# Optimization experiments

Hardware: AMD Instinct MI355X
Metric: run time of the kernel (lower is better)

## Reference

```python
import jax, jax.numpy as jnp
import numpy as np

IN_FEATURES = 2048
OUT_FEATURES = 2048
LOG_DIM = 11                      # ceil(log2(2048))
BUTTERFLY_DIM = 2 ** LOG_DIM      # 2048
MAX_BLOCKS = BUTTERFLY_DIM // 2   # 1024 (layer 0 has the most blocks)
BATCH = 16384


def setup_inputs() -> dict:
    key = jax.random.key(0)
    ks = jax.random.split(key, 5)
    x = jax.random.normal(ks[0], (BATCH, IN_FEATURES), dtype=jnp.float32)
    # Linear weights stored torch-style: [out, in]
    w_in = jax.random.normal(ks[1], (BUTTERFLY_DIM, IN_FEATURES), dtype=jnp.float32) * 0.02
    w_out = jax.random.normal(ks[2], (OUT_FEATURES, BUTTERFLY_DIM), dtype=jnp.float32) * 0.02
    b_out = jnp.zeros((OUT_FEATURES,), dtype=jnp.float32)
    # Per-stage rotation params: theta = rand*0.01, a=cos(theta), b=sin(theta).
    # Stage l uses num_blocks = BUTTERFLY_DIM // 2^(l+1) entries; pad to MAX_BLOCKS.
    theta = jax.random.uniform(ks[3], (LOG_DIM, MAX_BLOCKS), dtype=jnp.float32) * 0.01
    a_pad = jnp.cos(theta)
    b_pad = jnp.sin(theta)
    return {"x": x, "w_in": w_in, "w_out": w_out, "b_out": b_out,
            "a_pad": a_pad, "b_pad": b_pad}


def _butterfly(x, a_pad, b_pad):
    # x: [B, BUTTERFLY_DIM]
    B = x.shape[0]
    for l in range(LOG_DIM):
        block_size = 2 ** l
        num_blocks = BUTTERFLY_DIM // (2 * block_size)
        a = a_pad[l, :num_blocks][None, :, None]  # [1, nb, 1]
        b = b_pad[l, :num_blocks][None, :, None]
        xv = x.reshape(B, num_blocks, 2, block_size)
        x0 = xv[:, :, 0, :]
        x1 = xv[:, :, 1, :]
        top = a * x0 + b * x1
        bot = -b * x0 + a * x1
        x = jnp.stack([top, bot], axis=2).reshape(B, BUTTERFLY_DIM)
    return x


def reference(x, w_in, w_out, b_out, a_pad, b_pad):
    h = x @ w_in.T                      # [B, BUTTERFLY_DIM]
    h = _butterfly(h, a_pad, b_pad)
    return h @ w_out.T + b_out          # [B, OUT_FEATURES]
```

## Files before the change

kernel.cpp:

```cpp
#include <hip/hip_runtime.h>
#include <hip/hip_bf16.h>

using bf16 = __hip_bfloat16;
using bf16x8 = __attribute__((ext_vector_type(8))) __bf16;
using f32x4 = __attribute__((ext_vector_type(4))) float;

typedef const __attribute__((address_space(1))) void* gas_ptr;
typedef __attribute__((address_space(3))) void* las_ptr;
#define LOAD_LDS16(g, l) \
    __builtin_amdgcn_global_load_lds((gas_ptr)(const void*)(g), (las_ptr)(void*)(l), 16, 0, 0)

#define LOG_DIM 11
#define BDIM 2048
#define NFEAT 2048
#define BATCH 16384

__global__ __launch_bounds__(256) void cvt_fp32_bf16(const float* __restrict__ in,
                                                     bf16* __restrict__ out) {
    size_t i = ((size_t)blockIdx.x * 256 + threadIdx.x) * 8;
    float4 v0 = *(const float4*)(in + i);
    float4 v1 = *(const float4*)(in + i + 4);
    union { bf16 h[8]; int4 v; } u;
    u.h[0] = __float2bfloat16(v0.x); u.h[1] = __float2bfloat16(v0.y);
    u.h[2] = __float2bfloat16(v0.z); u.h[3] = __float2bfloat16(v0.w);
    u.h[4] = __float2bfloat16(v1.x); u.h[5] = __float2bfloat16(v1.y);
    u.h[6] = __float2bfloat16(v1.z); u.h[7] = __float2bfloat16(v1.w);
    *(int4*)(out + i) = u.v;
}

__global__ __launch_bounds__(256) void butterfly_wout(const float* __restrict__ W,
                                                      const float* __restrict__ a_pad,
                                                      const float* __restrict__ b_pad,
                                                      bf16* __restrict__ out) {
    __shared__ float v[BDIM];
    const int o = blockIdx.x;
    const int t = threadIdx.x;
    const float* row = W + (size_t)o * BDIM;
    for (int i = t; i < BDIM / 4; i += 256)
        ((float4*)v)[i] = ((const float4*)row)[i];
    __syncthreads();
    for (int l = LOG_DIM - 1; l >= 0; --l) {
        const int bs = 1 << l;
        #pragma unroll
        for (int pp = 0; pp < 4; ++pp) {
            int p = t + pp * 256;
            int j = p >> l;
            int s = p & (bs - 1);
            int i0 = (j << (l + 1)) | s;
            int i1 = i0 + bs;
            float a = a_pad[l * (BDIM / 2) + j];
            float b = b_pad[l * (BDIM / 2) + j];
            float x0 = v[i0], x1 = v[i1];
            v[i0] = a * x0 - b * x1;
            v[i1] = b * x0 + a * x1;
        }
        __syncthreads();
    }
    union { bf16 h[8]; int4 vv; } u;
    #pragma unroll
    for (int j = 0; j < 8; ++j) u.h[j] = __float2bfloat16(v[t * 8 + j]);
    *(int4*)(out + (size_t)o * BDIM + t * 8) = u.vv;
}

__global__ __launch_bounds__(256) void transpose_cvt(const float* __restrict__ in,
                                                     bf16* __restrict__ out) {
    __shared__ float tile[32][33];
    const int bx = blockIdx.x, by = blockIdx.y;
    const int tx = threadIdx.x & 31, ty = threadIdx.x >> 5;
    #pragma unroll
    for (int r = ty; r < 32; r += 8)
        tile[r][tx] = in[(size_t)(by * 32 + r) * NFEAT + bx * 32 + tx];
    __syncthreads();
    #pragma unroll
    for (int r = ty; r < 32; r += 8)
        out[(size_t)(bx * 32 + r) * NFEAT + by * 32 + tx] = __float2bfloat16(tile[tx][r]);
}

__global__ __launch_bounds__(256, 2) void gemm_bt_splitk(const bf16* __restrict__ A,
                                                         const bf16* __restrict__ Bt,
                                                         bf16* __restrict__ Cpart) {
    constexpr int BM = 128, BN = 128, BK = 32;
    constexpr int LDA = 2048, KLEN = 512, NN = 2048;
    __shared__ bf16 sA[BM * BK];
    __shared__ bf16 sB[BN * BK];

    const int kz = blockIdx.z;
    A += kz * KLEN;
    Bt += kz * KLEN;
    bf16* C = Cpart + (size_t)kz * NN * NN;

    const int tid = threadIdx.x;
    const int wave = tid >> 6;
    const int lane = tid & 63;
    const int wr = wave >> 1;
    const int wc = wave & 1;

    const int mBase = blockIdx.y * BM;
    const int nBase = blockIdx.x * BN;

    const int r0 = tid >> 2, c0 = tid & 3;
    const int r1 = (256 + tid) >> 2;

    const bf16* gA0 = A + (size_t)(mBase + r0) * LDA + c0 * 8;
    const bf16* gA1 = A + (size_t)(mBase + r1) * LDA + c0 * 8;
    const bf16* gB0 = Bt + (size_t)(nBase + r0) * LDA + c0 * 8;
    const bf16* gB1 = Bt + (size_t)(nBase + r1) * LDA + c0 * 8;

    char* lA0 = (char*)sA + (wave * 64) * 16;
    char* lA1 = (char*)sA + (256 + wave * 64) * 16;
    char* lB0 = (char*)sB + (wave * 64) * 16;
    char* lB1 = (char*)sB + (256 + wave * 64) * 16;

    f32x4 acc[4][4];
    #pragma unroll
    for (int i = 0; i < 4; ++i)
        #pragma unroll
        for (int j = 0; j < 4; ++j) acc[i][j] = (f32x4){0.f, 0.f, 0.f, 0.f};

    const int aRow = wr * 64 + (lane & 15);
    const int bRow = wc * 64 + (lane & 15);
    const int kOff = (lane >> 4) * 8;

    for (int k0 = 0; k0 < KLEN; k0 += BK) {
        LOAD_LDS16(gA0, lA0);
        LOAD_LDS16(gA1, lA1);
        LOAD_LDS16(gB0, lB0);
        LOAD_LDS16(gB1, lB1);
        gA0 += BK; gA1 += BK; gB0 += BK; gB1 += BK;
        __syncthreads();

        bf16x8 af[4], bfr[4];
        #pragma unroll
        for (int mf = 0; mf < 4; ++mf)
            af[mf] = *reinterpret_cast<const bf16x8*>(&sA[(aRow + mf * 16) * BK + kOff]);
        #pragma unroll
        for (int nf = 0; nf < 4; ++nf)
            bfr[nf] = *reinterpret_cast<const bf16x8*>(&sB[(bRow + nf * 16) * BK + kOff]);
        #pragma unroll
        for (int mf = 0; mf < 4; ++mf)
            #pragma unroll
            for (int nf = 0; nf < 4; ++nf)
                acc[mf][nf] = __builtin_amdgcn_mfma_f32_16x16x32_bf16(
                    af[mf], bfr[nf], acc[mf][nf], 0, 0, 0);
        __syncthreads();
    }

    const int cRow0 = mBase + wr * 64 + (lane >> 4) * 4;
    const int cCol0 = nBase + wc * 64 + (lane & 15);
    #pragma unroll
    for (int mf = 0; mf < 4; ++mf)
        #pragma unroll
        for (int nf = 0; nf < 4; ++nf)
            #pragma unroll
            for (int r = 0; r < 4; ++r)
                C[(size_t)(cRow0 + mf * 16 + r) * NN + cCol0 + nf * 16] =
                    __float2bfloat16(acc[mf][nf][r]);
}

__global__ __launch_bounds__(256) void addcvt4(const bf16* __restrict__ p,
                                               bf16* __restrict__ out) {
    size_t i = ((size_t)blockIdx.x * 256 + threadIdx.x) * 8;
    constexpr size_t STRIDE = (size_t)2048 * 2048;
    float s[8];
    #pragma unroll
    for (int j = 0; j < 8; ++j) s[j] = 0.f;
    #pragma unroll
    for (int z = 0; z < 4; ++z) {
        union { bf16 h[8]; int4 v; } a;
        a.v = *(const int4*)(p + z * STRIDE + i);
        #pragma unroll
        for (int j = 0; j < 8; ++j) s[j] += __bfloat162float(a.h[j]);
    }
    union { bf16 h[8]; int4 v; } o;
    #pragma unroll
    for (int j = 0; j < 8; ++j) o.h[j] = __float2bfloat16(s[j]);
    *(int4*)(out + i) = o.v;
}

#define GK 2048
#define LDS_SLOT 65536
#define LDS_BOFF 32768
#define LDS_KH 16384

__global__ __launch_bounds__(512, 2) void gemm256(const bf16* __restrict__ A,
                                                  const bf16* __restrict__ Bt,
                                                  const float* __restrict__ bias,
                                                  float* __restrict__ C) {
    __shared__ __align__(16) char lds[131072];

    const int tid = threadIdx.x;
    const int wave = tid >> 6, lane = tid & 63;
    const int l15 = lane & 15, kc = lane >> 4;
    const int wm = wave >> 2, wn = wave & 3;

    const int bid = blockIdx.x;
    const int swz = (bid & 7) * 64 + (bid >> 3);
    const int bm = swz >> 3, bn = swz & 7;
    const int mBase = bm * 256, nBase = bn * 256;

    const int c_log = tid ^ ((tid >> 3) & 3);
    const int srow = c_log >> 2, skc = c_log & 3;
    const bf16* gA = A + (size_t)(mBase + srow) * GK + skc * 8;
    const bf16* gB = Bt + (size_t)(nBase + srow) * GK + skc * 8;
    const int stgBase = wave * 1024;

    const int kcx = kc ^ ((l15 >> 1) & 3);
    const int aoff = wm * 8192 + l15 * 64 + kcx * 16;
    const int boff = LDS_BOFF + wn * 4096 + l15 * 64 + kcx * 16;

    f32x4 acc[8][4];
    #pragma unroll
    for (int i = 0; i < 8; ++i)
        #pragma unroll
        for (int j = 0; j < 4; ++j) acc[i][j] = (f32x4){0.f, 0.f, 0.f, 0.f};
    bf16x8 bfr[4];

#define STG(GSRC, LDSC, KT, KH) do {                                        \
    const bf16* _g = (GSRC) + (KT) * 64 + (KH) * 32;                        \
    LOAD_LDS16(_g, lds + (LDSC) + stgBase);                                 \
    LOAD_LDS16(_g + (size_t)128 * GK, lds + (LDSC) + stgBase + 8192);       \
} while (0)

    STG(gA, 0 * LDS_SLOT + 0, 0, 0);
    STG(gB, 0 * LDS_SLOT + LDS_BOFF + 0, 0, 0);
    STG(gA, 0 * LDS_SLOT + LDS_KH, 0, 1);
    STG(gB, 0 * LDS_SLOT + LDS_BOFF + LDS_KH, 0, 1);
    STG(gA, 1 * LDS_SLOT + 0, 1, 0);
    STG(gB, 1 * LDS_SLOT + LDS_BOFF + 0, 1, 0);
    STG(gB, 1 * LDS_SLOT + LDS_BOFF + LDS_KH, 1, 1);
    asm volatile("s_waitcnt vmcnt(6)");
    __builtin_amdgcn_s_barrier();

#define PHASE(SLOT, KH, MH, SGSRC, SLDS, SKT, SKH, DOVM) do {               \
    const int _rb = (SLOT) * LDS_SLOT + (KH) * LDS_KH;                      \
    bf16x8 _a[4];                                                           \
    _Pragma("unroll")                                                       \
    for (int _mf = 0; _mf < 4; ++_mf)                                       \
        _a[_mf] = *(const bf16x8*)(lds + _rb + aoff + (MH) * 4096 + _mf * 1024); \
    if (!(MH)) {                                                            \
        _Pragma("unroll")                                                   \
        for (int _nf = 0; _nf < 4; ++_nf)                                   \
            bfr[_nf] = *(const bf16x8*)(lds + _rb + boff + _nf * 1024);     \
    }                                                                       \
    STG(SGSRC, SLDS, SKT, SKH);                                             \
    if (DOVM) asm volatile("s_waitcnt vmcnt(6)");                           \
    __builtin_amdgcn_s_barrier();                                           \
    asm volatile("s_waitcnt lgkmcnt(0)");                                   \
    __builtin_amdgcn_s_setprio(1);                                          \
    _Pragma("unroll")                                                       \
    for (int _mf = 0; _mf < 4; ++_mf)                                       \
        _Pragma("unroll")                                                   \
        for (int _nf = 0; _nf < 4; ++_nf)                                   \
            acc[(MH) * 4 + _mf][_nf] = __builtin_amdgcn_mfma_f32_16x16x32_bf16( \
                _a[_mf], bfr[_nf], acc[(MH) * 4 + _mf][_nf], 0, 0, 0);      \
    __builtin_amdgcn_s_setprio(0);                                          \
    __builtin_amdgcn_s_barrier();                                           \
} while (0)

    for (int it = 0; it < 16; ++it) {
        const int t0 = 2 * it;
        const int t1 = (t0 + 1) & 31, t2 = (t0 + 2) & 31, t3 = (t0 + 3) & 31;
        PHASE(0, 0, 0, gA, 1 * LDS_SLOT + LDS_KH,            t1, 1, 0);
        PHASE(0, 0, 1, gB, 0 * LDS_SLOT + LDS_BOFF,          t2, 0, 0);
        PHASE(0, 1, 0, gA, 0 * LDS_SLOT + 0,                 t2, 0, 0);
        PHASE(0, 1, 1, gB, 0 * LDS_SLOT + LDS_BOFF + LDS_KH, t2, 1, 1);
        PHASE(1, 0, 0, gA, 0 * LDS_SLOT + LDS_KH,            t2, 1, 0);
        PHASE(1, 0, 1, gB, 1 * LDS_SLOT + LDS_BOFF,          t3, 0, 0);
        PHASE(1, 1, 0, gA, 1 * LDS_SLOT + 0,                 t3, 0, 0);
        PHASE(1, 1, 1, gB, 1 * LDS_SLOT + LDS_BOFF + LDS_KH, t3, 1, 1);
    }

    const int cRow0 = mBase + wm * 128 + (lane >> 4) * 4;
    const int cCol0 = nBase + wn * 64 + l15;
    float bv[4];
    #pragma unroll
    for (int nf = 0; nf < 4; ++nf) bv[nf] = bias[cCol0 + nf * 16];
    #pragma unroll
    for (int Mf = 0; Mf < 8; ++Mf)
        #pragma unroll
        for (int nf = 0; nf < 4; ++nf)
            #pragma unroll
            for (int r = 0; r < 4; ++r)
                C[(size_t)(cRow0 + Mf * 16 + r) * GK + cCol0 + nf * 16] =
                    acc[Mf][nf][r] + bv[nf];
#undef PHASE
#undef STG
}

extern "C" void kernel_launch(void* const* d_in, const int* in_sizes, int n_in,
                              void* d_out, int out_size, void* d_ws, size_t ws_size,
                              hipStream_t stream) {
    const float* x     = (const float*)d_in[0];
    const float* w_in  = (const float*)d_in[1];
    const float* w_out = (const float*)d_in[2];
    const float* b_out = (const float*)d_in[3];
    const float* a_pad = (const float*)d_in[4];
    const float* b_pad = (const float*)d_in[5];
    float* out = (float*)d_out;

    char* ws = (char*)d_ws;
    bf16* x_bf  = (bf16*)ws;
    bf16* woutb = (bf16*)(ws + (size_t)67108864);
    bf16* wint  = (bf16*)(ws + (size_t)75497472);
    bf16* mcomb = (bf16*)(ws + (size_t)83886080);

    bf16* part = (bf16*)d_out;

    cvt_fp32_bf16<<<dim3(BATCH * NFEAT / (256 * 8)), dim3(256), 0, stream>>>(x, x_bf);
    butterfly_wout<<<dim3(NFEAT), dim3(256), 0, stream>>>(w_out, a_pad, b_pad, woutb);
    transpose_cvt<<<dim3(NFEAT / 32, BDIM / 32), dim3(256), 0, stream>>>(w_in, wint);
    gemm_bt_splitk<<<dim3(NFEAT / 128, BDIM / 128, 4), dim3(256), 0, stream>>>(
        woutb, wint, part);
    addcvt4<<<dim3(NFEAT * BDIM / (256 * 8)), dim3(256), 0, stream>>>(part, mcomb);
    gemm256<<<dim3((BATCH / 256) * (NFEAT / 256)), dim3(512), 0, stream>>>(
        x_bf, mcomb, b_out, out);
}
```

Before: 223.7 us.

## Merge prep kernels and double-buffer LDS fragment reads in main GEMM

The butterfly-on-w_out and w_in transpose kernels are merged into one launch, and the x fp32-to-bf16 conversion is interleaved with the split-K weight GEMM in a second launch. This cuts launch count and lets the memory-bound conversion overlap with the compute-bound small GEMM. The main 256x256 GEMM now reads the next phase's A/B fragments from LDS into alternate register sets while the current MFMAs run, removing the lgkmcnt(0) stall before each MFMA block. This adds register pressure and relies on barrier placement to keep the prefetched LDS reads valid.

```diff
diff --git a/kernel.cpp b/kernel.cpp
--- a/kernel.cpp
+++ b/kernel.cpp
@@ -15,88 +15,91 @@
 #define NFEAT 2048
 #define BATCH 16384
 
-__global__ __launch_bounds__(256) void cvt_fp32_bf16(const float* __restrict__ in,
-                                                     bf16* __restrict__ out) {
-    size_t i = ((size_t)blockIdx.x * 256 + threadIdx.x) * 8;
-    float4 v0 = *(const float4*)(in + i);
-    float4 v1 = *(const float4*)(in + i + 4);
-    union { bf16 h[8]; int4 v; } u;
-    u.h[0] = __float2bfloat16(v0.x); u.h[1] = __float2bfloat16(v0.y);
-    u.h[2] = __float2bfloat16(v0.z); u.h[3] = __float2bfloat16(v0.w);
-    u.h[4] = __float2bfloat16(v1.x); u.h[5] = __float2bfloat16(v1.y);
-    u.h[6] = __float2bfloat16(v1.z); u.h[7] = __float2bfloat16(v1.w);
-    *(int4*)(out + i) = u.v;
-}
-
-__global__ __launch_bounds__(256) void butterfly_wout(const float* __restrict__ W,
-                                                      const float* __restrict__ a_pad,
-                                                      const float* __restrict__ b_pad,
-                                                      bf16* __restrict__ out) {
+__global__ __launch_bounds__(256) void prep1(const float* __restrict__ w_out,
+                                             const float* __restrict__ a_pad,
+                                             const float* __restrict__ b_pad,
+                                             const float* __restrict__ w_in,
+                                             bf16* __restrict__ woutb,
+                                             bf16* __restrict__ wint) {
     __shared__ float v[BDIM];
-    const int o = blockIdx.x;
+    __shared__ float tile[32][33];
     const int t = threadIdx.x;
-    const float* row = W + (size_t)o * BDIM;
-    for (int i = t; i < BDIM / 4; i += 256)
-        ((float4*)v)[i] = ((const float4*)row)[i];
-    __syncthreads();
-    for (int l = LOG_DIM - 1; l >= 0; --l) {
-        const int bs = 1 << l;
-        #pragma unroll
-        for (int pp = 0; pp < 4; ++pp) {
-            int p = t + pp * 256;
-            int j = p >> l;
-            int s = p & (bs - 1);
-            int i0 = (j << (l + 1)) | s;
-            int i1 = i0 + bs;
-            float a = a_pad[l * (BDIM / 2) + j];
-            float b = b_pad[l * (BDIM / 2) + j];
-            float x0 = v[i0], x1 = v[i1];
-            v[i0] = a * x0 - b * x1;
-            v[i1] = b * x0 + a * x1;
+    if (blockIdx.x < 2048) {
+        const int o = blockIdx.x;
+        const float* row = w_out + (size_t)o * BDIM;
+        for (int i = t; i < BDIM / 4; i += 256)
+            ((float4*)v)[i] = ((const float4*)row)[i];
+        __syncthreads();
+        for (int l = LOG_DIM - 1; l >= 0; --l) {
+            #pragma unroll
+            for (int pp = 0; pp < 4; ++pp) {
+                int p = t + pp * 256;
+                int j = p >> l;
+                int s = p & ((1 << l) - 1);
+                int i0 = (j << (l + 1)) | s;
+                int i1 = i0 + (1 << l);
+                float a = a_pad[l * (BDIM / 2) + j];
+                float b = b_pad[l * (BDIM / 2) + j];
+                float x0 = v[i0], x1 = v[i1];
+                v[i0] = a * x0 - b * x1;
+                v[i1] = b * x0 + a * x1;
+            }
+            __syncthreads();
         }
+        union { bf16 h[8]; int4 vv; } u;
+        #pragma unroll
+        for (int j = 0; j < 8; ++j) u.h[j] = __float2bfloat16(v[t * 8 + j]);
+        *(int4*)(woutb + (size_t)o * BDIM + t * 8) = u.vv;
+    } else {
+        const int b = blockIdx.x - 2048;
+        const int bx = b & 63, by = b >> 6;
+        const int tx = t & 31, ty = t >> 5;
+        #pragma unroll
+        for (int r = ty; r < 32; r += 8)
+            tile[r][tx] = w_in[(size_t)(by * 32 + r) * NFEAT + bx * 32 + tx];
         __syncthreads();
-    }
-    union { bf16 h[8]; int4 vv; } u;
-    #pragma unroll
-    for (int j = 0; j < 8; ++j) u.h[j] = __float2bfloat16(v[t * 8 + j]);
-    *(int4*)(out + (size_t)o * BDIM + t * 8) = u.vv;
-}
-
-__global__ __launch_bounds__(256) void transpose_cvt(const float* __restrict__ in,
-                                                     bf16* __restrict__ out) {
-    __shared__ float tile[32][33];
-    const int bx = blockIdx.x, by = blockIdx.y;
-    const int tx = threadIdx.x & 31, ty = threadIdx.x >> 5;
-    #pragma unroll
-    for (int r = ty; r < 32; r += 8)
-        tile[r][tx] = in[(size_t)(by * 32 + r) * NFEAT + bx * 32 + tx];
-    __syncthreads();
-    #pragma unroll
-    for (int r = ty; r < 32; r += 8)
-        out[(size_t)(bx * 32 + r) * NFEAT + by * 32 + tx] = __float2bfloat16(tile[tx][r]);
-}
-
-__global__ __launch_bounds__(256, 2) void gemm_bt_splitk(const bf16* __restrict__ A,
-                                                         const bf16* __restrict__ Bt,
-                                                         bf16* __restrict__ Cpart) {
-    constexpr int BM = 128, BN = 128, BK = 32;
-    constexpr int LDA = 2048, KLEN = 512, NN = 2048;
-    __shared__ bf16 sA[BM * BK];
-    __shared__ bf16 sB[BN * BK];
-
-    const int kz = blockIdx.z;
-    A += kz * KLEN;
-    Bt += kz * KLEN;
+        #pragma unroll
+        for (int r = ty; r < 32; r += 8)
+            wint[(size_t)(bx * 32 + r) * NFEAT + by * 32 + tx] = __float2bfloat16(tile[tx][r]);
+    }
+}
+
+__global__ __launch_bounds__(256, 2) void prep2(const bf16* __restrict__ Aw,
+                                                const bf16* __restrict__ Btw,
+                                                bf16* __restrict__ Cpart,
+                                                const float* __restrict__ x,
+                                                bf16* __restrict__ x_bf) {
+    __shared__ bf16 sA[128 * 32];
+    __shared__ bf16 sB[128 * 32];
+    const int tid = threadIdx.x;
+
+    if (blockIdx.x & 1) {
+        const int vb = blockIdx.x >> 1;
+        #pragma unroll
+        for (int it = 0; it < 16; ++it) {
+            size_t i = ((size_t)vb * 16 + it) * 2048 + tid * 8;
+            float4 v0 = *(const float4*)(x + i);
+            float4 v1 = *(const float4*)(x + i + 4);
+            union { bf16 h[8]; int4 v; } u;
+            u.h[0] = __float2bfloat16(v0.x); u.h[1] = __float2bfloat16(v0.y);
+            u.h[2] = __float2bfloat16(v0.z); u.h[3] = __float2bfloat16(v0.w);
+            u.h[4] = __float2bfloat16(v1.x); u.h[5] = __float2bfloat16(v1.y);
+            u.h[6] = __float2bfloat16(v1.z); u.h[7] = __float2bfloat16(v1.w);
+            *(int4*)(x_bf + i) = u.v;
+        }
+        return;
+    }
+
+    constexpr int BK = 32, LDA = 2048, KLEN = 512, NN = 2048;
+    const int sk = blockIdx.x >> 1;
+    const int bx = sk & 15, by = (sk >> 4) & 15, kz = sk >> 8;
+    const bf16* A = Aw + kz * KLEN;
+    const bf16* Bt = Btw + kz * KLEN;
     bf16* C = Cpart + (size_t)kz * NN * NN;
 
-    const int tid = threadIdx.x;
-    const int wave = tid >> 6;
-    const int lane = tid & 63;
-    const int wr = wave >> 1;
-    const int wc = wave & 1;
-
-    const int mBase = blockIdx.y * BM;
-    const int nBase = blockIdx.x * BN;
+    const int wave = tid >> 6, lane = tid & 63;
+    const int wr = wave >> 1, wc = wave & 1;
+    const int mBase = by * 128, nBase = bx * 128;
 
     const int r0 = tid >> 2, c0 = tid & 3;
     const int r1 = (256 + tid) >> 2;
@@ -128,7 +131,6 @@
         LOAD_LDS16(gB1, lB1);
         gA0 += BK; gA1 += BK; gB0 += BK; gB1 += BK;
         __syncthreads();
-
         bf16x8 af[4], bfr[4];
         #pragma unroll
         for (int mf = 0; mf < 4; ++mf)
@@ -213,12 +215,25 @@
     for (int i = 0; i < 8; ++i)
         #pragma unroll
         for (int j = 0; j < 4; ++j) acc[i][j] = (f32x4){0.f, 0.f, 0.f, 0.f};
-    bf16x8 bfr[4];
+
+    bf16x8 Aa[4], Ab[4], Ba[4], Bb[4];
 
 #define STG(GSRC, LDSC, KT, KH) do {                                        \
     const bf16* _g = (GSRC) + (KT) * 64 + (KH) * 32;                        \
     LOAD_LDS16(_g, lds + (LDSC) + stgBase);                                 \
     LOAD_LDS16(_g + (size_t)128 * GK, lds + (LDSC) + stgBase + 8192);       \
+} while (0)
+
+#define READP(AN, BN, SLOT, KH, MH, DOB) do {                               \
+    const int _rb = (SLOT) * LDS_SLOT + (KH) * LDS_KH;                      \
+    _Pragma("unroll")                                                       \
+    for (int _f = 0; _f < 4; ++_f)                                          \
+        AN[_f] = *(const bf16x8*)(lds + _rb + aoff + (MH) * 4096 + _f * 1024); \
+    if (DOB) {                                                              \
+        _Pragma("unroll")                                                   \
+        for (int _f = 0; _f < 4; ++_f)                                      \
+            BN[_f] = *(const bf16x8*)(lds + _rb + boff + _f * 1024);        \
+    }                                                                       \
 } while (0)
 
     STG(gA, 0 * LDS_SLOT + 0, 0, 0);
@@ -230,29 +245,20 @@
     STG(gB, 1 * LDS_SLOT + LDS_BOFF + LDS_KH, 1, 1);
     asm volatile("s_waitcnt vmcnt(6)");
     __builtin_amdgcn_s_barrier();
-
-#define PHASE(SLOT, KH, MH, SGSRC, SLDS, SKT, SKH, DOVM) do {               \
-    const int _rb = (SLOT) * LDS_SLOT + (KH) * LDS_KH;                      \
-    bf16x8 _a[4];                                                           \
-    _Pragma("unroll")                                                       \
-    for (int _mf = 0; _mf < 4; ++_mf)                                       \
-        _a[_mf] = *(const bf16x8*)(lds + _rb + aoff + (MH) * 4096 + _mf * 1024); \
-    if (!(MH)) {                                                            \
-        _Pragma("unroll")                                                   \
-        for (int _nf = 0; _nf < 4; ++_nf)                                   \
-            bfr[_nf] = *(const bf16x8*)(lds + _rb + boff + _nf * 1024);     \
-    }                                                                       \
+    READP(Aa, Ba, 0, 0, 0, 1);
+
+#define PH(CURA, CURB, NXTA, NXTB, MH, RS, RKH, RMH, RDOB, SGSRC, SLDS, SKT, SKH, DOVM) do { \
     STG(SGSRC, SLDS, SKT, SKH);                                             \
     if (DOVM) asm volatile("s_waitcnt vmcnt(6)");                           \
     __builtin_amdgcn_s_barrier();                                           \
-    asm volatile("s_waitcnt lgkmcnt(0)");                                   \
+    READP(NXTA, NXTB, RS, RKH, RMH, RDOB);                                  \
     __builtin_amdgcn_s_setprio(1);                                          \
     _Pragma("unroll")                                                       \
     for (int _mf = 0; _mf < 4; ++_mf)                                       \
         _Pragma("unroll")                                                   \
         for (int _nf = 0; _nf < 4; ++_nf)                                   \
             acc[(MH) * 4 + _mf][_nf] = __builtin_amdgcn_mfma_f32_16x16x32_bf16( \
-                _a[_mf], bfr[_nf], acc[(MH) * 4 + _mf][_nf], 0, 0, 0);      \
+                CURA[_mf], CURB[_nf], acc[(MH) * 4 + _mf][_nf], 0, 0, 0);   \
     __builtin_amdgcn_s_setprio(0);                                          \
     __builtin_amdgcn_s_barrier();                                           \
 } while (0)
@@ -260,14 +266,14 @@
     for (int it = 0; it < 16; ++it) {
         const int t0 = 2 * it;
         const int t1 = (t0 + 1) & 31, t2 = (t0 + 2) & 31, t3 = (t0 + 3) & 31;
-        PHASE(0, 0, 0, gA, 1 * LDS_SLOT + LDS_KH,            t1, 1, 0);
-        PHASE(0, 0, 1, gB, 0 * LDS_SLOT + LDS_BOFF,          t2, 0, 0);
-        PHASE(0, 1, 0, gA, 0 * LDS_SLOT + 0,                 t2, 0, 0);
-        PHASE(0, 1, 1, gB, 0 * LDS_SLOT + LDS_BOFF + LDS_KH, t2, 1, 1);
-        PHASE(1, 0, 0, gA, 0 * LDS_SLOT + LDS_KH,            t2, 1, 0);
-        PHASE(1, 0, 1, gB, 1 * LDS_SLOT + LDS_BOFF,          t3, 0, 0);
-        PHASE(1, 1, 0, gA, 1 * LDS_SLOT + 0,                 t3, 0, 0);
-        PHASE(1, 1, 1, gB, 1 * LDS_SLOT + LDS_BOFF + LDS_KH, t3, 1, 1);
+        PH(Aa, Ba, Ab, Bb, 0, 0, 0, 1, 0, gA, 1 * LDS_SLOT + LDS_KH,            t1, 1, 0);
+        PH(Ab, Ba, Aa, Bb, 1, 0, 1, 0, 1, gB, 0 * LDS_SLOT + LDS_BOFF,          t2, 0, 0);
+        PH(Aa, Bb, Ab, Ba, 0, 0, 1, 1, 0, gA, 0 * LDS_SLOT + 0,                 t2, 0, 0);
+        PH(Ab, Bb, Aa, Ba, 1, 1, 0, 0, 1, gB, 0 * LDS_SLOT + LDS_BOFF + LDS_KH, t2, 1, 1);
+        PH(Aa, Ba, Ab, Bb, 0, 1, 0, 1, 0, gA, 0 * LDS_SLOT + LDS_KH,            t2, 1, 0);
+        PH(Ab, Ba, Aa, Bb, 1, 1, 1, 0, 1, gB, 1 * LDS_SLOT + LDS_BOFF,          t3, 0, 0);
+        PH(Aa, Bb, Ab, Ba, 0, 1, 1, 1, 0, gA, 1 * LDS_SLOT + 0,                 t3, 0, 0);
+        PH(Ab, Bb, Aa, Ba, 1, 0, 0, 0, 1, gB, 1 * LDS_SLOT + LDS_BOFF + LDS_KH, t3, 1, 1);
     }
 
     const int cRow0 = mBase + wm * 128 + (lane >> 4) * 4;
@@ -283,7 +289,8 @@
             for (int r = 0; r < 4; ++r)
                 C[(size_t)(cRow0 + Mf * 16 + r) * GK + cCol0 + nf * 16] =
                     acc[Mf][nf][r] + bv[nf];
-#undef PHASE
+#undef PH
+#undef READP
 #undef STG
 }
 
@@ -306,11 +313,8 @@
 
     bf16* part = (bf16*)d_out;
 
-    cvt_fp32_bf16<<<dim3(BATCH * NFEAT / (256 * 8)), dim3(256), 0, stream>>>(x, x_bf);
-    butterfly_wout<<<dim3(NFEAT), dim3(256), 0, stream>>>(w_out, a_pad, b_pad, woutb);
-    transpose_cvt<<<dim3(NFEAT / 32, BDIM / 32), dim3(256), 0, stream>>>(w_in, wint);
-    gemm_bt_splitk<<<dim3(NFEAT / 128, BDIM / 128, 4), dim3(256), 0, stream>>>(
-        woutb, wint, part);
+    prep1<<<dim3(6144), dim3(256), 0, stream>>>(w_out, a_pad, b_pad, w_in, woutb, wint);
+    prep2<<<dim3(2048), dim3(256), 0, stream>>>(woutb, wint, part, x, x_bf);
     addcvt4<<<dim3(NFEAT * BDIM / (256 * 8)), dim3(256), 0, stream>>>(part, mcomb);
     gemm256<<<dim3((BATCH / 256) * (NFEAT / 256)), dim3(512), 0, stream>>>(
         x_bf, mcomb, b_out, out);
```

Measured after the change: 205.7 us. 8.1% less time.
